# Kernel tuning notes

Hardware: AMD Instinct MI355X
Metric: run time of the kernel (lower is better)

Reference implementation:

```python
import jax, jax.numpy as jnp
import numpy as np

B, S, D, H, R, N, KR = 2, 2048, 1024, 16, 256, 8, 128
DH = D // H
EPS = 1e-5


def setup_inputs() -> dict:
    key = jax.random.key(0)
    ks = jax.random.split(key, 20)
    sm = lambda k, n: jax.nn.softmax(jax.random.normal(k, (B, S, n), jnp.float32), axis=-1)
    return {
        "x": jax.random.normal(ks[0], (B, S, D), jnp.float32),
        "fqk_w_Q": sm(ks[1], N),
        "fqk_w_K": sm(ks[2], N),
        "fv_w": sm(ks[3], N),
        "rqk_w_Q": sm(ks[4], N),
        "rqk_w_K": sm(ks[5], N),
        "rv_w": sm(ks[6], N),
        "feature_know_w": sm(ks[7], N),
        "restore_know_w": sm(ks[8], N),
        "f_qk": jax.random.normal(ks[9], (N, D, R), jnp.float32) * 0.02,
        "f_v": jax.random.normal(ks[10], (N, D, R), jnp.float32) * 0.02,
        "r_qk": jax.random.normal(ks[11], (N, R, D), jnp.float32) * 0.02,
        "r_v": jax.random.normal(ks[12], (N, R, D), jnp.float32) * 0.02,
        "f_know": jax.random.normal(ks[13], (N, D, KR), jnp.float32) * 0.02,
        "r_know": jax.random.normal(ks[14], (N, KR, D), jnp.float32) * 0.02,
        "W_O": jax.random.normal(ks[15], (D, D), jnp.float32) * 0.02,
        "ln1_g": jnp.ones((D,), jnp.float32),
        "ln1_b": jnp.zeros((D,), jnp.float32),
        "ln2_g": jnp.ones((D,), jnp.float32),
        "ln2_b": jnp.zeros((D,), jnp.float32),
    }


def _layernorm(x, g, b):
    m = jnp.mean(x, axis=-1, keepdims=True)
    v = jnp.mean(jnp.square(x - m), axis=-1, keepdims=True)
    return (x - m) * jax.lax.rsqrt(v + EPS) * g + b


def _feature(x, neurons, w):
    # fused form of einsum('bsd,ndr->bsnr') + einsum('bsnr,bsn->bsr')
    return jnp.einsum('bsd,bsn,ndr->bsr', x, w, neurons)


def _restore(h, neurons, w):
    # fused form of einsum('bsr,nrd->bsnd') + einsum('bsnd,bsn->bsd')
    return jnp.einsum('bsr,bsn,nrd->bsd', h, w, neurons)


def _causal_sdpa(q, k, v):
    # q,k,v: [B,H,S,DH]
    scores = jnp.einsum('bhqd,bhkd->bhqk', q, k) / jnp.sqrt(jnp.float32(DH))
    mask = jnp.tril(jnp.ones((S, S), bool))
    scores = jnp.where(mask, scores, jnp.finfo(scores.dtype).min)
    p = jax.nn.softmax(scores, axis=-1)
    return jnp.einsum('bhqk,bhkd->bhqd', p, v)


def _block(x, fqk_w_Q, fqk_w_K, fv_w, rqk_w_Q, rqk_w_K, rv_w,
           feature_know_w, restore_know_w, f_qk, f_v, r_qk, r_v,
           f_know, r_know, W_O, ln1_g, ln1_b, ln2_g, ln2_b):
    nx = _layernorm(x, ln1_g, ln1_b)
    h_q = _feature(nx, f_qk, fqk_w_Q)
    h_k = _feature(nx, f_qk, fqk_w_K)
    h_v = _feature(nx, f_v, fv_w)
    Q = _restore(h_q, r_qk, rqk_w_Q)
    K = _restore(h_k, r_qk, rqk_w_K)
    V = _restore(h_v, r_v, rv_w)
    to_heads = lambda t: t.reshape(B, S, H, DH).transpose(0, 2, 1, 3)
    attn = _causal_sdpa(to_heads(Q), to_heads(K), to_heads(V))
    attn = attn.transpose(0, 2, 1, 3).reshape(B, S, D)
    attn_out = attn @ W_O.T  # nn.Linear(d_model,d_model,bias=False)
    x = x + attn_out
    nx2 = _layernorm(x, ln2_g, ln2_b)
    h = _feature(nx2, f_know, feature_know_w)
    know_out = _restore(h, r_know, restore_know_w)
    return x + know_out


def reference(x, fqk_w_Q, fqk_w_K, fv_w, rqk_w_Q, rqk_w_K, rv_w,
              feature_know_w, restore_know_w, f_qk, f_v, r_qk, r_v,
              f_know, r_know, W_O, ln1_g, ln1_b, ln2_g, ln2_b):
    return _block(x, fqk_w_Q, fqk_w_K, fv_w, rqk_w_Q, rqk_w_K, rv_w,
                  feature_know_w, restore_know_w, f_qk, f_v, r_qk, r_v,
                  f_know, r_know, W_O, ln1_g, ln1_b, ln2_g, ln2_b)
```

## Files before the change

kernel.cpp:

```cpp
#include <hip/hip_runtime.h>
#include <hip/hip_bf16.h>


typedef __bf16 bf16_t;
typedef __bf16 bf16x8 __attribute__((ext_vector_type(8)));
typedef float f32x4 __attribute__((ext_vector_type(4)));

#define B_DIM 2
#define S_LEN 2048
#define D_DIM 1024
#define H_NUM 16
#define DH 64
#define N_NEU 8
#define R_DIM 256
#define KR_DIM 128
#define ROWS (B_DIM * S_LEN)

static __device__ __forceinline__ void gl_lds16(const void* g, void* l)
{
    __builtin_amdgcn_global_load_lds(
        (__attribute__((address_space(1))) void*)(g),
        (__attribute__((address_space(3))) void*)(l), 16, 0, 0);
}

__global__ __launch_bounds__(256)
void tcast_kernel(const float* __restrict__ in, bf16_t* __restrict__ out, int I, int J)
{
    __shared__ float t[32][33];
    const int bJ = blockIdx.x * 32, bI = blockIdx.y * 32;
    const size_t boff = (size_t)blockIdx.z * I * J;
    const int tx = threadIdx.x, ty = threadIdx.y;
#pragma unroll
    for (int i = 0; i < 4; i++)
        t[ty * 4 + i][tx] = in[boff + (size_t)(bI + ty * 4 + i) * J + bJ + tx];
    __syncthreads();
#pragma unroll
    for (int i = 0; i < 4; i++)
        out[boff + (size_t)(bJ + ty * 4 + i) * I + bI + tx] = (bf16_t)t[tx][ty * 4 + i];
}

__global__ __launch_bounds__(256)
void tbf_kernel(const bf16_t* __restrict__ in, bf16_t* __restrict__ out, int I, int J)
{
    __shared__ bf16_t t[32][33];
    const int bJ = blockIdx.x * 32, bI = blockIdx.y * 32;
    const size_t boff = (size_t)blockIdx.z * I * J;
    const int tx = threadIdx.x, ty = threadIdx.y;
#pragma unroll
    for (int i = 0; i < 4; i++)
        t[ty * 4 + i][tx] = in[boff + (size_t)(bI + ty * 4 + i) * J + bJ + tx];
    __syncthreads();
#pragma unroll
    for (int i = 0; i < 4; i++)
        out[boff + (size_t)(bJ + ty * 4 + i) * I + bI + tx] = t[tx][ty * 4 + i];
}

__global__ __launch_bounds__(256)
void cast_kernel(const float* __restrict__ in, bf16_t* __restrict__ out, int n4)
{
    int i = blockIdx.x * 256 + threadIdx.x;
    if (i < n4) {
        float4 v = ((const float4*)in)[i];
        bf16_t* op = out + (size_t)i * 4;
        op[0] = (bf16_t)v.x; op[1] = (bf16_t)v.y; op[2] = (bf16_t)v.z; op[3] = (bf16_t)v.w;
    }
}

__global__ __launch_bounds__(256)
void ln_kernel(const float* __restrict__ x, const float* __restrict__ g,
               const float* __restrict__ beta, bf16_t* __restrict__ out)
{
    __shared__ float red[4];
    const int row = blockIdx.x;
    const int tid = threadIdx.x;
    float4 v = *(const float4*)&x[(size_t)row * D_DIM + tid * 4];

    float s = v.x + v.y + v.z + v.w;
#pragma unroll
    for (int o = 32; o; o >>= 1) s += __shfl_down(s, o);
    if ((tid & 63) == 0) red[tid >> 6] = s;
    __syncthreads();
    float mean = (red[0] + red[1] + red[2] + red[3]) * (1.f / D_DIM);
    __syncthreads();

    float dx = v.x - mean, dy = v.y - mean, dz = v.z - mean, dw = v.w - mean;
    float q = dx * dx + dy * dy + dz * dz + dw * dw;
#pragma unroll
    for (int o = 32; o; o >>= 1) q += __shfl_down(q, o);
    if ((tid & 63) == 0) red[tid >> 6] = q;
    __syncthreads();
    float var = (red[0] + red[1] + red[2] + red[3]) * (1.f / D_DIM);
    float rstd = rsqrtf(var + 1e-5f);

    float4 gv = *(const float4*)&g[tid * 4];
    float4 bv = *(const float4*)&beta[tid * 4];
    bf16_t* op = out + (size_t)row * D_DIM + tid * 4;
    op[0] = (bf16_t)(dx * rstd * gv.x + bv.x);
    op[1] = (bf16_t)(dy * rstd * gv.y + bv.y);
    op[2] = (bf16_t)(dz * rstd * gv.z + bv.z);
    op[3] = (bf16_t)(dw * rstd * gv.w + bv.w);
}

__global__ __launch_bounds__(256)
void ln2x_kernel(const float* __restrict__ x, const float* __restrict__ P0,
                 const float* __restrict__ P1, const float* __restrict__ g,
                 const float* __restrict__ beta, float* __restrict__ outf,
                 bf16_t* __restrict__ outn)
{
    __shared__ float red[4];
    const int row = blockIdx.x;
    const int tid = threadIdx.x;
    const size_t base = (size_t)row * D_DIM + tid * 4;
    float4 v  = *(const float4*)&x[base];
    float4 p0 = *(const float4*)&P0[base];
    float4 p1 = *(const float4*)&P1[base];
    v.x += p0.x + p1.x; v.y += p0.y + p1.y; v.z += p0.z + p1.z; v.w += p0.w + p1.w;
    *(float4*)&outf[base] = v;

    float s = v.x + v.y + v.z + v.w;
#pragma unroll
    for (int o = 32; o; o >>= 1) s += __shfl_down(s, o);
    if ((tid & 63) == 0) red[tid >> 6] = s;
    __syncthreads();
    float mean = (red[0] + red[1] + red[2] + red[3]) * (1.f / D_DIM);
    __syncthreads();

    float dx = v.x - mean, dy = v.y - mean, dz = v.z - mean, dw = v.w - mean;
    float q = dx * dx + dy * dy + dz * dz + dw * dw;
#pragma unroll
    for (int o = 32; o; o >>= 1) q += __shfl_down(q, o);
    if ((tid & 63) == 0) red[tid >> 6] = q;
    __syncthreads();
    float var = (red[0] + red[1] + red[2] + red[3]) * (1.f / D_DIM);
    float rstd = rsqrtf(var + 1e-5f);

    float4 gv = *(const float4*)&g[tid * 4];
    float4 bv = *(const float4*)&beta[tid * 4];
    bf16_t* op = outn + base;
    op[0] = (bf16_t)(dx * rstd * gv.x + bv.x);
    op[1] = (bf16_t)(dy * rstd * gv.y + bv.y);
    op[2] = (bf16_t)(dz * rstd * gv.z + bv.z);
    op[3] = (bf16_t)(dw * rstd * gv.w + bv.w);
}

__global__ __launch_bounds__(256)
void wsf_kernel(const bf16_t* __restrict__ y,
                const float* __restrict__ wfQ, const float* __restrict__ wrQ,
                const float* __restrict__ wfK, const float* __restrict__ wrK,
                const float* __restrict__ wfV, const float* __restrict__ wrV,
                bf16_t* __restrict__ sq, bf16_t* __restrict__ sk, bf16_t* __restrict__ sv)
{
    const int r = threadIdx.x;
    const int row = blockIdx.x;
    const bf16_t* yrow = y + (size_t)row * 4096;
    const float* fQ = wfQ + row * N_NEU;
    const float* fK = wfK + row * N_NEU;
    const float* fV = wfV + row * N_NEU;
    float aQ = 0.f, aK = 0.f, aV = 0.f;
#pragma unroll
    for (int n = 0; n < N_NEU; n++) {
        float yq = (float)yrow[n * R_DIM + r];
        float yv = (float)yrow[2048 + n * R_DIM + r];
        aQ += fQ[n] * yq;
        aK += fK[n] * yq;
        aV += fV[n] * yv;
    }
    const float* rQ = wrQ + row * N_NEU;
    const float* rK = wrK + row * N_NEU;
    const float* rV = wrV + row * N_NEU;
    const size_t rb = (size_t)row * 2048;
#pragma unroll
    for (int n = 0; n < N_NEU; n++) {
        sq[rb + n * R_DIM + r] = (bf16_t)(rQ[n] * aQ);
        sk[rb + n * R_DIM + r] = (bf16_t)(rK[n] * aK);
        sv[rb + n * R_DIM + r] = (bf16_t)(rV[n] * aV);
    }
}

__global__ __launch_bounds__(256)
void ws2_kernel(const float* __restrict__ P0, const float* __restrict__ P1,
                const float* __restrict__ wf, const float* __restrict__ wr,
                bf16_t* __restrict__ sout)
{
    const int lr = threadIdx.x >> 7;
    const int r  = threadIdx.x & 127;
    const int row = blockIdx.x * 2 + lr;
    const size_t rb = (size_t)row * (N_NEU * KR_DIM);
    const float* wfp = wf + row * N_NEU;
    const float* wrp = wr + row * N_NEU;
    float acc = 0.f;
#pragma unroll
    for (int n = 0; n < N_NEU; n++) {
        size_t i = rb + n * KR_DIM + r;
        acc += wfp[n] * (P0[i] + P1[i]);
    }
    bf16_t* srow = sout + rb;
#pragma unroll
    for (int n = 0; n < N_NEU; n++) srow[n * KR_DIM + r] = (bf16_t)(wrp[n] * acc);
}

template<int EPI>
__global__ __launch_bounds__(256)
void gemm_kernel(const bf16_t* __restrict__ A, const bf16_t* __restrict__ Bt,
                 const bf16_t* __restrict__ Bt2, int splitMy,
                 void* Cout, const float* resid, int M, int N, int K)
{
    __shared__ bf16_t As[3][128][32];
    __shared__ bf16_t Bs[3][128][32];
    const int tid = threadIdx.x;
    const int l = tid & 63, w = tid >> 6;
    const int wr = w >> 1, wc = w & 1;

    const int nbxy = gridDim.x * gridDim.y;
    int bid = blockIdx.y * gridDim.x + blockIdx.x;
    if ((nbxy & 7) == 0) bid = (bid & 7) * (nbxy >> 3) + (bid >> 3);
    const int bx = bid % gridDim.x, by = bid / gridDim.x;

    const int m0 = by * 128, n0 = bx * 128;
    const bf16_t* Bsel = (by < splitMy) ? Bt : Bt2;

    int kbeg = 0, kend = K;
    if constexpr (EPI == 2) { const int half = K >> 1; kbeg = blockIdx.z * half; kend = kbeg + half; }

    const int srow = l >> 2;
    const int scol = (l & 3) * 8;
    const bf16_t* Ag0 = A    + (size_t)(m0 + w * 32 + srow) * K + scol;
    const bf16_t* Ag1 = Ag0 + (size_t)16 * K;
    const bf16_t* Bg0 = Bsel + (size_t)(n0 + w * 32 + srow) * K + scol;
    const bf16_t* Bg1 = Bg0 + (size_t)16 * K;

    auto stage = [&](int buf, int k0) {
        char* Asb = (char*)&As[buf][0][0] + w * 2048;
        char* Bsb = (char*)&Bs[buf][0][0] + w * 2048;
        gl_lds16(Ag0 + k0, Asb);
        gl_lds16(Ag1 + k0, Asb + 1024);
        gl_lds16(Bg0 + k0, Bsb);
        gl_lds16(Bg1 + k0, Bsb + 1024);
    };

    f32x4 acc[4][4];
    const f32x4 zero = {0.f, 0.f, 0.f, 0.f};
#pragma unroll
    for (int i = 0; i < 4; i++)
#pragma unroll
        for (int j = 0; j < 4; j++) acc[i][j] = zero;

    const int fr = l & 15;
    const int fk = (l >> 4) * 8;

    stage(0, kbeg);
    stage(1, kbeg + 32);

    const int nK = (kend - kbeg) >> 5;
    for (int it = 0; it < nK; ++it) {
        if (it + 1 < nK) {
            asm volatile("s_waitcnt vmcnt(4)" ::: "memory");
        } else {
            asm volatile("s_waitcnt vmcnt(0)" ::: "memory");
        }
        __builtin_amdgcn_s_barrier();
        __builtin_amdgcn_sched_barrier(0);

        const int cur = it % 3;
        bf16x8 af[4], bv[4];
#pragma unroll
        for (int i = 0; i < 4; i++) af[i] = *(const bf16x8*)&As[cur][wr * 64 + i * 16 + fr][fk];
#pragma unroll
        for (int i = 0; i < 4; i++) bv[i] = *(const bf16x8*)&Bs[cur][wc * 64 + i * 16 + fr][fk];

        if (it + 2 < nK) stage((it + 2) % 3, kbeg + (it + 2) * 32);

        __builtin_amdgcn_s_setprio(1);
#pragma unroll
        for (int mi = 0; mi < 4; mi++)
#pragma unroll
            for (int ni = 0; ni < 4; ni++)
                acc[mi][ni] = __builtin_amdgcn_mfma_f32_16x16x32_bf16(af[mi], bv[ni], acc[mi][ni], 0, 0, 0);
        __builtin_amdgcn_s_setprio(0);
    }

    const int orow = (l >> 4) * 4;
    const int ocol = l & 15;
#pragma unroll
    for (int mi = 0; mi < 4; mi++)
#pragma unroll
        for (int ni = 0; ni < 4; ni++)
#pragma unroll
            for (int j = 0; j < 4; j++) {
                int row = m0 + wr * 64 + mi * 16 + orow + j;
                int col = n0 + wc * 64 + ni * 16 + ocol;
                size_t idx = (size_t)row * N + col;
                if constexpr (EPI == 0) {
                    ((bf16_t*)Cout)[idx] = (bf16_t)acc[mi][ni][j];
                } else if constexpr (EPI == 1) {
                    ((float*)Cout)[idx] = acc[mi][ni][j] + resid[idx];
                } else {
                    ((float*)Cout)[(size_t)blockIdx.z * M * N + idx] = acc[mi][ni][j];
                }
            }
}

__global__ __launch_bounds__(256)
void fa_kernel(const bf16_t* __restrict__ Q, const bf16_t* __restrict__ K,
               const bf16_t* __restrict__ Vt, bf16_t* __restrict__ O)
{
    __shared__ bf16_t Ks[64][72];
    __shared__ bf16_t Vs[64][72];
    __shared__ bf16_t Ps[4][16][72];

    const int tid = threadIdx.x;
    const int l = tid & 63, w = tid >> 6;

    const int bid  = blockIdx.x;
    const int xcd  = bid & 7;
    const int slot = bid >> 3;
    const int head = slot & 3;
    const int jq   = slot >> 2;
    const int bh   = xcd * 4 + head;
    const int b = bh >> 4, h = bh & 15;

    const bf16_t* Qp = Q + (size_t)b * S_LEN * D_DIM + h * DH;
    const bf16_t* Kp = K + (size_t)b * S_LEN * D_DIM + h * DH;
    const bf16_t* Vp = Vt + (size_t)b * D_DIM * S_LEN + (size_t)h * DH * S_LEN;

    const int fr = l & 15, fg = l >> 4, fk = fg * 8;
    const int srow = tid >> 2;
    const int scol = (tid & 3) * 16;
    const bf16_t* Kst = Kp + (size_t)srow * D_DIM + scol;
    const bf16_t* Vst = Vp + (size_t)srow * S_LEN + scol;

    bf16x8 ones8;
#pragma unroll
    for (int i = 0; i < 8; i++) ones8[i] = (bf16_t)1.f;

    const f32x4 zero = {0.f, 0.f, 0.f, 0.f};
    const float C_LOG2 = 0.125f * 1.44269504f;

    for (int pass = 0; pass < 2; ++pass) {
        const int qb = pass ? jq : (31 - jq);
        const int q0 = qb * 64;
        const int nt = qb + 1;

        bf16x8 qf[2];
#pragma unroll
        for (int ks = 0; ks < 2; ks++)
            qf[ks] = *(const bf16x8*)(Qp + (size_t)(q0 + w * 16 + fr) * D_DIM + ks * 32 + fk);

        f32x4 o[4];
        f32x4 la = zero;
        float m_r[4];
#pragma unroll
        for (int j = 0; j < 4; j++) { o[j] = zero; m_r[j] = -1e30f; }

        uint4 kva = *(const uint4*)(Kst);
        uint4 kvb = *(const uint4*)(Kst + 8);
        uint4 vva = *(const uint4*)(Vst);
        uint4 vvb = *(const uint4*)(Vst + 8);

        for (int t = 0; t < nt; t++) {
            const int k0 = t * 64;
            __syncthreads();
            *(uint4*)&Ks[srow][scol]     = kva;
            *(uint4*)&Ks[srow][scol + 8] = kvb;
            *(uint4*)&Vs[srow][scol]     = vva;
            *(uint4*)&Vs[srow][scol + 8] = vvb;
            __syncthreads();

            if (t + 1 < nt) {
                const int kn = k0 + 64;
                kva = *(const uint4*)(Kst + (size_t)kn * D_DIM);
                kvb = *(const uint4*)(Kst + (size_t)kn * D_DIM + 8);
                vva = *(const uint4*)(Vst + kn);
                vvb = *(const uint4*)(Vst + kn + 8);
            }

            f32x4 sc[4];
#pragma unroll
            for (int ni = 0; ni < 4; ni++) sc[ni] = zero;
            __builtin_amdgcn_s_setprio(1);
#pragma unroll
            for (int ks = 0; ks < 2; ks++) {
#pragma unroll
                for (int ni = 0; ni < 4; ni++) {
                    bf16x8 kf = *(const bf16x8*)&Ks[ni * 16 + fr][ks * 32 + fk];
                    sc[ni] = __builtin_amdgcn_mfma_f32_16x16x32_bf16(qf[ks], kf, sc[ni], 0, 0, 0);
                }
            }
            __builtin_amdgcn_s_setprio(0);

            float p[4][4];
            if (t == qb) {
#pragma unroll
                for (int ni = 0; ni < 4; ni++) {
                    const int key = k0 + ni * 16 + fr;
#pragma unroll
                    for (int j = 0; j < 4; j++) {
                        const int qg = q0 + w * 16 + fg * 4 + j;
                        p[ni][j] = (key <= qg) ? sc[ni][j] * C_LOG2 : -1e30f;
                    }
                }
            } else {
#pragma unroll
                for (int ni = 0; ni < 4; ni++)
#pragma unroll
                    for (int j = 0; j < 4; j++)
                        p[ni][j] = sc[ni][j] * C_LOG2;
            }

#pragma unroll
            for (int j = 0; j < 4; j++) {
                float rmax = fmaxf(fmaxf(p[0][j], p[1][j]), fmaxf(p[2][j], p[3][j]));
#pragma unroll
                for (int d = 1; d < 16; d <<= 1) rmax = fmaxf(rmax, __shfl_xor(rmax, d));
                if (rmax > m_r[j] + 8.f) {
                    float scale = exp2f(m_r[j] - rmax);
                    la[j] *= scale;
#pragma unroll
                    for (int nc = 0; nc < 4; nc++) o[nc][j] *= scale;
                    m_r[j] = rmax;
                }
#pragma unroll
                for (int ni = 0; ni < 4; ni++)
                    p[ni][j] = exp2f(p[ni][j] - m_r[j]);
            }

#pragma unroll
            for (int ni = 0; ni < 4; ni++)
#pragma unroll
                for (int j = 0; j < 4; j++)
                    Ps[w][fg * 4 + j][ni * 16 + fr] = (bf16_t)p[ni][j];

            __builtin_amdgcn_s_setprio(1);
#pragma unroll
            for (int ks = 0; ks < 2; ks++) {
                bf16x8 pa = *(const bf16x8*)&Ps[w][fr][ks * 32 + fk];
                la = __builtin_amdgcn_mfma_f32_16x16x32_bf16(pa, ones8, la, 0, 0, 0);
#pragma unroll
                for (int nc = 0; nc < 4; nc++) {
                    bf16x8 vf = *(const bf16x8*)&Vs[nc * 16 + fr][fk + ks * 32];
                    o[nc] = __builtin_amdgcn_mfma_f32_16x16x32_bf16(pa, vf, o[nc], 0, 0, 0);
                }
            }
            __builtin_amdgcn_s_setprio(0);
        }

#pragma unroll
        for (int j = 0; j < 4; j++) {
            const float inv = 1.f / la[j];
            const int q = q0 + w * 16 + fg * 4 + j;
            bf16_t* op = O + (size_t)(b * S_LEN + q) * D_DIM + h * DH;
#pragma unroll
            for (int nc = 0; nc < 4; nc++)
                op[nc * 16 + fr] = (bf16_t)(o[nc][j] * inv);
        }
    }
}

extern "C" void kernel_launch(void* const* d_in, const int* in_sizes, int n_in,
                              void* d_out, int out_size, void* d_ws, size_t ws_size,
                              hipStream_t stream)
{
    const float* x      = (const float*)d_in[0];
    const float* fqk_wQ = (const float*)d_in[1];
    const float* fqk_wK = (const float*)d_in[2];
    const float* fv_w   = (const float*)d_in[3];
    const float* rqk_wQ = (const float*)d_in[4];
    const float* rqk_wK = (const float*)d_in[5];
    const float* rv_w   = (const float*)d_in[6];
    const float* fkn_w  = (const float*)d_in[7];
    const float* rkn_w  = (const float*)d_in[8];
    const float* f_qk   = (const float*)d_in[9];
    const float* f_v    = (const float*)d_in[10];
    const float* r_qk   = (const float*)d_in[11];
    const float* r_v    = (const float*)d_in[12];
    const float* f_know = (const float*)d_in[13];
    const float* r_know = (const float*)d_in[14];
    const float* W_O    = (const float*)d_in[15];
    const float* ln1g   = (const float*)d_in[16];
    const float* ln1b   = (const float*)d_in[17];
    const float* ln2g   = (const float*)d_in[18];
    const float* ln2b   = (const float*)d_in[19];
    float* out_f = (float*)d_out;
    (void)ws_size; (void)in_sizes; (void)n_in; (void)out_size;

    char* ws = (char*)d_ws;
    const size_t MB = 1024 * 1024;
    bf16_t* rqkT   = (bf16_t*)(ws + 0 * MB);
    bf16_t* rvT    = (bf16_t*)(ws + 4 * MB);
    bf16_t* rknT   = (bf16_t*)(ws + 8 * MB);
    bf16_t* woB    = (bf16_t*)(ws + 10 * MB);
    bf16_t* fknT   = (bf16_t*)(ws + 12 * MB);
    bf16_t* buf_nx = (bf16_t*)(ws + 14 * MB);
    bf16_t* buf_y  = (bf16_t*)(ws + 22 * MB);
    char*   buf_s  = ws + 54 * MB;
    bf16_t* fqkT   = (bf16_t*)(buf_s);
    bf16_t* fvT    = (bf16_t*)(buf_s + 4 * MB);
    bf16_t* s_q    = (bf16_t*)(buf_s);
    bf16_t* s_k    = (bf16_t*)(buf_s) + (size_t)4096 * 2048;
    bf16_t* s_v    = (bf16_t*)(buf_s) + (size_t)8192 * 2048;
    bf16_t* attn   = (bf16_t*)(buf_s);
    float*  P0     = (float*)(buf_s + 16 * MB);
    float*  P0k    = (float*)(buf_s);
    float*  P1k    = (float*)(buf_s + 16 * MB);
    bf16_t* sk2    = (bf16_t*)(buf_s + 32 * MB);
    bf16_t* Qb     = buf_y;
    bf16_t* Kb     = buf_y + (size_t)4096 * 1024;
    bf16_t* Vb     = buf_y + (size_t)8192 * 1024;
    bf16_t* Vt     = buf_nx;

    const dim3 blk256(256), blkT(32, 8);

    tcast_kernel<<<dim3(R_DIM / 32, D_DIM / 32, N_NEU), blkT, 0, stream>>>(f_qk, fqkT, D_DIM, R_DIM);
    tcast_kernel<<<dim3(R_DIM / 32, D_DIM / 32, N_NEU), blkT, 0, stream>>>(f_v, fvT, D_DIM, R_DIM);
    tcast_kernel<<<dim3(KR_DIM / 32, D_DIM / 32, N_NEU), blkT, 0, stream>>>(f_know, fknT, D_DIM, KR_DIM);
    tcast_kernel<<<dim3(D_DIM / 32, 2048 / 32, 1), blkT, 0, stream>>>(r_qk, rqkT, 2048, D_DIM);
    tcast_kernel<<<dim3(D_DIM / 32, 2048 / 32, 1), blkT, 0, stream>>>(r_v, rvT, 2048, D_DIM);
    tcast_kernel<<<dim3(D_DIM / 32, 1024 / 32, 1), blkT, 0, stream>>>(r_know, rknT, 1024, D_DIM);
    cast_kernel<<<dim3(1024 * 1024 / 4 / 256), blk256, 0, stream>>>(W_O, woB, 1024 * 1024 / 4);

    ln_kernel<<<dim3(ROWS), blk256, 0, stream>>>(x, ln1g, ln1b, buf_nx);

    gemm_kernel<0><<<dim3(32, 32), blk256, 0, stream>>>(buf_nx, fqkT, fqkT, 1 << 30, buf_y, nullptr, 4096, 4096, 1024);

    wsf_kernel<<<dim3(ROWS), blk256, 0, stream>>>(buf_y, fqk_wQ, rqk_wQ, fqk_wK, rqk_wK, fv_w, rv_w, s_q, s_k, s_v);

    gemm_kernel<0><<<dim3(8, 96), blk256, 0, stream>>>((bf16_t*)buf_s, rqkT, rvT, 64, buf_y, nullptr, 12288, 1024, 2048);

    tbf_kernel<<<dim3(D_DIM / 32, S_LEN / 32, B_DIM), blkT, 0, stream>>>(Vb, Vt, S_LEN, D_DIM);

    fa_kernel<<<dim3(512), blk256, 0, stream>>>(Qb, Kb, Vt, attn);

    gemm_kernel<2><<<dim3(8, 32, 2), blk256, 0, stream>>>(attn, woB, woB, 1 << 30, P0, nullptr, 4096, 1024, 1024);

    ln2x_kernel<<<dim3(ROWS), blk256, 0, stream>>>(x, P0, P0 + (size_t)4096 * 1024, ln2g, ln2b, out_f, buf_nx);

    gemm_kernel<2><<<dim3(8, 32, 2), blk256, 0, stream>>>(buf_nx, fknT, fknT, 1 << 30, P0k, nullptr, 4096, 1024, 1024);

    ws2_kernel<<<dim3(ROWS / 2), blk256, 0, stream>>>(P0k, P1k, fkn_w, rkn_w, sk2);

    gemm_kernel<1><<<dim3(8, 32), blk256, 0, stream>>>(sk2, rknT, rknT, 1 << 30, d_out, out_f, 4096, 1024, 1024);
}
```

Before: 317.9 us.

## Widen flash-attention key tile to 128 and store split-K partials in bf16

The attention kernel now processes 128 keys per iteration instead of 64. This halves the number of loop iterations, barriers and online-softmax rescales per query block, at the cost of more LDS and registers per block. Separately, the split-K GEMM partial outputs (attention projection and knowledge feature) are written and read as bf16 instead of fp32, which halves that intermediate traffic. Rounding the partial sums to bf16 before they are summed adds numerical error.

```diff
diff --git a/kernel.cpp b/kernel.cpp
--- a/kernel.cpp
+++ b/kernel.cpp
@@ -3,6 +3,7 @@
 
 
 typedef __bf16 bf16_t;
+typedef __bf16 bf16x4 __attribute__((ext_vector_type(4)));
 typedef __bf16 bf16x8 __attribute__((ext_vector_type(8)));
 typedef float f32x4 __attribute__((ext_vector_type(4)));
 
@@ -102,8 +103,8 @@
 }
 
 __global__ __launch_bounds__(256)
-void ln2x_kernel(const float* __restrict__ x, const float* __restrict__ P0,
-                 const float* __restrict__ P1, const float* __restrict__ g,
+void ln2x_kernel(const float* __restrict__ x, const bf16_t* __restrict__ P0,
+                 const bf16_t* __restrict__ P1, const float* __restrict__ g,
                  const float* __restrict__ beta, float* __restrict__ outf,
                  bf16_t* __restrict__ outn)
 {
@@ -112,9 +113,12 @@
     const int tid = threadIdx.x;
     const size_t base = (size_t)row * D_DIM + tid * 4;
     float4 v  = *(const float4*)&x[base];
-    float4 p0 = *(const float4*)&P0[base];
-    float4 p1 = *(const float4*)&P1[base];
-    v.x += p0.x + p1.x; v.y += p0.y + p1.y; v.z += p0.z + p1.z; v.w += p0.w + p1.w;
+    bf16x4 p0 = *(const bf16x4*)&P0[base];
+    bf16x4 p1 = *(const bf16x4*)&P1[base];
+    v.x += (float)p0[0] + (float)p1[0];
+    v.y += (float)p0[1] + (float)p1[1];
+    v.z += (float)p0[2] + (float)p1[2];
+    v.w += (float)p0[3] + (float)p1[3];
     *(float4*)&outf[base] = v;
 
     float s = v.x + v.y + v.z + v.w;
@@ -178,7 +182,7 @@
 }
 
 __global__ __launch_bounds__(256)
-void ws2_kernel(const float* __restrict__ P0, const float* __restrict__ P1,
+void ws2_kernel(const bf16_t* __restrict__ P0, const bf16_t* __restrict__ P1,
                 const float* __restrict__ wf, const float* __restrict__ wr,
                 bf16_t* __restrict__ sout)
 {
@@ -192,7 +196,7 @@
 #pragma unroll
     for (int n = 0; n < N_NEU; n++) {
         size_t i = rb + n * KR_DIM + r;
-        acc += wfp[n] * (P0[i] + P1[i]);
+        acc += wfp[n] * ((float)P0[i] + (float)P1[i]);
     }
     bf16_t* srow = sout + rb;
 #pragma unroll
@@ -295,7 +299,7 @@
                 } else if constexpr (EPI == 1) {
                     ((float*)Cout)[idx] = acc[mi][ni][j] + resid[idx];
                 } else {
-                    ((float*)Cout)[(size_t)blockIdx.z * M * N + idx] = acc[mi][ni][j];
+                    ((bf16_t*)Cout)[(size_t)blockIdx.z * M * N + idx] = (bf16_t)acc[mi][ni][j];
                 }
             }
 }
@@ -304,9 +308,9 @@
 void fa_kernel(const bf16_t* __restrict__ Q, const bf16_t* __restrict__ K,
                const bf16_t* __restrict__ Vt, bf16_t* __restrict__ O)
 {
-    __shared__ bf16_t Ks[64][72];
-    __shared__ bf16_t Vs[64][72];
-    __shared__ bf16_t Ps[4][16][72];
+    __shared__ bf16_t Ks[128][72];
+    __shared__ bf16_t Vs[64][136];
+    __shared__ bf16_t Ps[4][16][136];
 
     const int tid = threadIdx.x;
     const int l = tid & 63, w = tid >> 6;
@@ -339,7 +343,7 @@
     for (int pass = 0; pass < 2; ++pass) {
         const int qb = pass ? jq : (31 - jq);
         const int q0 = qb * 64;
-        const int nt = qb + 1;
+        const int nt = (qb >> 1) + 1;
 
         bf16x8 qf[2];
 #pragma unroll
@@ -354,62 +358,86 @@
 
         uint4 kva = *(const uint4*)(Kst);
         uint4 kvb = *(const uint4*)(Kst + 8);
+        uint4 kvc = *(const uint4*)(Kst + (size_t)64 * D_DIM);
+        uint4 kvd = *(const uint4*)(Kst + (size_t)64 * D_DIM + 8);
         uint4 vva = *(const uint4*)(Vst);
         uint4 vvb = *(const uint4*)(Vst + 8);
+        uint4 vvc = *(const uint4*)(Vst + 64);
+        uint4 vvd = *(const uint4*)(Vst + 72);
 
         for (int t = 0; t < nt; t++) {
-            const int k0 = t * 64;
+            const int k0 = t * 128;
             __syncthreads();
-            *(uint4*)&Ks[srow][scol]     = kva;
-            *(uint4*)&Ks[srow][scol + 8] = kvb;
-            *(uint4*)&Vs[srow][scol]     = vva;
-            *(uint4*)&Vs[srow][scol + 8] = vvb;
+            *(uint4*)&Ks[srow][scol]          = kva;
+            *(uint4*)&Ks[srow][scol + 8]      = kvb;
+            *(uint4*)&Ks[64 + srow][scol]     = kvc;
+            *(uint4*)&Ks[64 + srow][scol + 8] = kvd;
+            *(uint4*)&Vs[srow][scol]          = vva;
+            *(uint4*)&Vs[srow][scol + 8]      = vvb;
+            *(uint4*)&Vs[srow][64 + scol]     = vvc;
+            *(uint4*)&Vs[srow][64 + scol + 8] = vvd;
             __syncthreads();
 
             if (t + 1 < nt) {
-                const int kn = k0 + 64;
+                const int kn = k0 + 128;
                 kva = *(const uint4*)(Kst + (size_t)kn * D_DIM);
                 kvb = *(const uint4*)(Kst + (size_t)kn * D_DIM + 8);
+                kvc = *(const uint4*)(Kst + (size_t)(kn + 64) * D_DIM);
+                kvd = *(const uint4*)(Kst + (size_t)(kn + 64) * D_DIM + 8);
                 vva = *(const uint4*)(Vst + kn);
                 vvb = *(const uint4*)(Vst + kn + 8);
+                vvc = *(const uint4*)(Vst + kn + 64);
+                vvd = *(const uint4*)(Vst + kn + 72);
             }
 
-            f32x4 sc[4];
-#pragma unroll
-            for (int ni = 0; ni < 4; ni++) sc[ni] = zero;
+            f32x4 sc[2][4];
+#pragma unroll
+            for (int s2 = 0; s2 < 2; s2++)
+#pragma unroll
+                for (int ni = 0; ni < 4; ni++) sc[s2][ni] = zero;
             __builtin_amdgcn_s_setprio(1);
 #pragma unroll
             for (int ks = 0; ks < 2; ks++) {
 #pragma unroll
-                for (int ni = 0; ni < 4; ni++) {
-                    bf16x8 kf = *(const bf16x8*)&Ks[ni * 16 + fr][ks * 32 + fk];
-                    sc[ni] = __builtin_amdgcn_mfma_f32_16x16x32_bf16(qf[ks], kf, sc[ni], 0, 0, 0);
-                }
+                for (int s2 = 0; s2 < 2; s2++)
+#pragma unroll
+                    for (int ni = 0; ni < 4; ni++) {
+                        bf16x8 kf = *(const bf16x8*)&Ks[s2 * 64 + ni * 16 + fr][ks * 32 + fk];
+                        sc[s2][ni] = __builtin_amdgcn_mfma_f32_16x16x32_bf16(qf[ks], kf, sc[s2][ni], 0, 0, 0);
+                    }
             }
             __builtin_amdgcn_s_setprio(0);
 
-            float p[4][4];
-            if (t == qb) {
-#pragma unroll
-                for (int ni = 0; ni < 4; ni++) {
-                    const int key = k0 + ni * 16 + fr;
-#pragma unroll
-                    for (int j = 0; j < 4; j++) {
-                        const int qg = q0 + w * 16 + fg * 4 + j;
-                        p[ni][j] = (key <= qg) ? sc[ni][j] * C_LOG2 : -1e30f;
+            float p[2][4][4];
+            if (t == nt - 1) {
+#pragma unroll
+                for (int s2 = 0; s2 < 2; s2++)
+#pragma unroll
+                    for (int ni = 0; ni < 4; ni++) {
+                        const int key = k0 + s2 * 64 + ni * 16 + fr;
+#pragma unroll
+                        for (int j = 0; j < 4; j++) {
+                            const int qg = q0 + w * 16 + fg * 4 + j;
+                            p[s2][ni][j] = (key <= qg) ? sc[s2][ni][j] * C_LOG2 : -1e30f;
+                        }
                     }
-                }
             } else {
 #pragma unroll
-                for (int ni = 0; ni < 4; ni++)
-#pragma unroll
-                    for (int j = 0; j < 4; j++)
-                        p[ni][j] = sc[ni][j] * C_LOG2;
+                for (int s2 = 0; s2 < 2; s2++)
+#pragma unroll
+                    for (int ni = 0; ni < 4; ni++)
+#pragma unroll
+                        for (int j = 0; j < 4; j++)
+                            p[s2][ni][j] = sc[s2][ni][j] * C_LOG2;
             }
 
 #pragma unroll
             for (int j = 0; j < 4; j++) {
-                float rmax = fmaxf(fmaxf(p[0][j], p[1][j]), fmaxf(p[2][j], p[3][j]));
+                float rmax = p[0][0][j];
+#pragma unroll
+                for (int s2 = 0; s2 < 2; s2++)
+#pragma unroll
+                    for (int ni = 0; ni < 4; ni++) rmax = fmaxf(rmax, p[s2][ni][j]);
 #pragma unroll
                 for (int d = 1; d < 16; d <<= 1) rmax = fmaxf(rmax, __shfl_xor(rmax, d));
                 if (rmax > m_r[j] + 8.f) {
@@ -420,24 +448,28 @@
                     m_r[j] = rmax;
                 }
 #pragma unroll
+                for (int s2 = 0; s2 < 2; s2++)
+#pragma unroll
+                    for (int ni = 0; ni < 4; ni++)
+                        p[s2][ni][j] = exp2f(p[s2][ni][j] - m_r[j]);
+            }
+
+#pragma unroll
+            for (int s2 = 0; s2 < 2; s2++)
+#pragma unroll
                 for (int ni = 0; ni < 4; ni++)
-                    p[ni][j] = exp2f(p[ni][j] - m_r[j]);
-            }
-
-#pragma unroll
-            for (int ni = 0; ni < 4; ni++)
-#pragma unroll
-                for (int j = 0; j < 4; j++)
-                    Ps[w][fg * 4 + j][ni * 16 + fr] = (bf16_t)p[ni][j];
+#pragma unroll
+                    for (int j = 0; j < 4; j++)
+                        Ps[w][fg * 4 + j][s2 * 64 + ni * 16 + fr] = (bf16_t)p[s2][ni][j];
 
             __builtin_amdgcn_s_setprio(1);
 #pragma unroll
-            for (int ks = 0; ks < 2; ks++) {
+            for (int ks = 0; ks < 4; ks++) {
                 bf16x8 pa = *(const bf16x8*)&Ps[w][fr][ks * 32 + fk];
                 la = __builtin_amdgcn_mfma_f32_16x16x32_bf16(pa, ones8, la, 0, 0, 0);
 #pragma unroll
                 for (int nc = 0; nc < 4; nc++) {
-                    bf16x8 vf = *(const bf16x8*)&Vs[nc * 16 + fr][fk + ks * 32];
+                    bf16x8 vf = *(const bf16x8*)&Vs[nc * 16 + fr][ks * 32 + fk];
                     o[nc] = __builtin_amdgcn_mfma_f32_16x16x32_bf16(pa, vf, o[nc], 0, 0, 0);
                 }
             }
@@ -499,9 +531,8 @@
     bf16_t* s_k    = (bf16_t*)(buf_s) + (size_t)4096 * 2048;
     bf16_t* s_v    = (bf16_t*)(buf_s) + (size_t)8192 * 2048;
     bf16_t* attn   = (bf16_t*)(buf_s);
-    float*  P0     = (float*)(buf_s + 16 * MB);
-    float*  P0k    = (float*)(buf_s);
-    float*  P1k    = (float*)(buf_s + 16 * MB);
+    bf16_t* P0     = (bf16_t*)(buf_s + 16 * MB);
+    bf16_t* P0k    = (bf16_t*)(buf_s);
     bf16_t* sk2    = (bf16_t*)(buf_s + 32 * MB);
     bf16_t* Qb     = buf_y;
     bf16_t* Kb     = buf_y + (size_t)4096 * 1024;
@@ -536,7 +567,7 @@
 
     gemm_kernel<2><<<dim3(8, 32, 2), blk256, 0, stream>>>(buf_nx, fknT, fknT, 1 << 30, P0k, nullptr, 4096, 1024, 1024);
 
-    ws2_kernel<<<dim3(ROWS / 2), blk256, 0, stream>>>(P0k, P1k, fkn_w, rkn_w, sk2);
+    ws2_kernel<<<dim3(ROWS / 2), blk256, 0, stream>>>(P0k, P0k + (size_t)4096 * 1024, fkn_w, rkn_w, sk2);
 
     gemm_kernel<1><<<dim3(8, 32), blk256, 0, stream>>>(sk2, rknT, rknT, 1 << 30, d_out, out_f, 4096, 1024, 1024);
 }
```

Result: faster. 302.5 us (-4.8%).
